# Kernel optimization log

Measured on AMD Instinct MI355X. Metric: run time of the kernel, lower is better.

## Reference

```python
import jax, jax.numpy as jnp
import numpy as np

B, N, M = 16, 4096, 1024
C2, C1 = 256, 128          # points2 channels (in_channel), points1 channels
MLP = [256, 256]
IN0 = C2 + C1              # use_points1=True concat


def setup_inputs() -> dict:
    key = jax.random.key(0)
    ks = jax.random.split(key, 8)
    inp = {
        "xyz1": jax.random.normal(ks[0], (B, 3, N), jnp.float32),
        "xyz2": jax.random.normal(ks[1], (B, 3, M), jnp.float32),
        "points1": jax.random.normal(ks[2], (B, C1, N), jnp.float32),
        "points2": jax.random.normal(ks[3], (B, C2, M), jnp.float32),
        # 1x1 Conv1d weights == dense matrices (out, in)
        "W1": jax.random.normal(ks[4], (MLP[0], IN0), jnp.float32) / np.sqrt(IN0),
        "b1": jnp.zeros((MLP[0],), jnp.float32),
        "W2": jax.random.normal(ks[5], (MLP[1], MLP[0]), jnp.float32) / np.sqrt(MLP[0]),
        "b2": jnp.zeros((MLP[1],), jnp.float32),
    }
    return inp


def _fp(xyz1, xyz2, points1, points2, W1, b1, W2, b2):
    # three_nn: squared pairwise distances via ||a||^2 + ||b||^2 - 2 a.b
    # xyz*: (B, 3, N/M)
    sq1 = jnp.sum(xyz1 * xyz1, axis=1)                 # (B, N)
    sq2 = jnp.sum(xyz2 * xyz2, axis=1)                 # (B, M)
    inner = jnp.einsum("bcn,bcm->bnm", xyz1, xyz2)     # (B, N, M)
    d2 = sq1[:, :, None] + sq2[:, None, :] - 2.0 * inner
    neg_d2, idx = jax.lax.top_k(-d2, 3)                # 3 smallest -> (B, N, 3)
    dist = jnp.sqrt(jnp.maximum(-neg_d2, 1e-20))       # Euclidean, like three_nn wrapper
    dist = jnp.maximum(dist, 1e-10)                    # torch.clamp_min
    recip = 1.0 / dist
    weight = recip / jnp.sum(recip, axis=2, keepdims=True)  # (B, N, 3)
    # three_interpolate: gather points2 at idx and weighted-sum
    gathered = jax.vmap(lambda p, i: p[:, i])(points2, idx)  # (B, C2, N, 3)
    interp = jnp.einsum("bcnk,bnk->bcn", gathered, weight)   # (B, C2, N)
    x = jnp.concatenate([interp, points1], axis=1)           # (B, C2+C1, N)
    # mlp_conv: 1x1 conv + relu (if_bn=False)
    x = jax.nn.relu(jnp.einsum("oc,bcn->bon", W1, x) + b1[None, :, None])
    x = jax.nn.relu(jnp.einsum("oc,bcn->bon", W2, x) + b2[None, :, None])
    return x


def reference(xyz1, xyz2, points1, points2, W1, b1, W2, b2):
    return _fp(xyz1, xyz2, points1, points2, W1, b1, W2, b2)
```

## Files before the change

### kernel.cpp

```cpp
#include <hip/hip_runtime.h>

#define B_  16
#define N_  4096
#define M_  1024
#define C1_ 128
#define C2_ 256
#define K0_ 384
#define O1_ 256
#define O2_ 256

typedef _Float16 half4  __attribute__((ext_vector_type(4)));
typedef _Float16 half8  __attribute__((ext_vector_type(8)));
typedef float    f32x4  __attribute__((ext_vector_type(4)));

__global__ __launch_bounds__(256)
void three_nn_kernel(const float* __restrict__ xyz1, const float* __restrict__ xyz2,
                     int* __restrict__ idxb, float* __restrict__ wb) {
    __shared__ float pts[8 * 516];
    int b = blockIdx.y;
    int t = threadIdx.x;
    {
        const float* src = xyz2 + (size_t)b * 3 * M_;
        int m0 = t * 4;
        f32x4 xv = *(const f32x4*)(src + m0);
        f32x4 yv = *(const f32x4*)(src + M_ + m0);
        f32x4 zv = *(const f32x4*)(src + 2 * M_ + m0);
        float* dst = pts + (m0 >> 7) * 516 + (m0 & 127) * 4;
#pragma unroll
        for (int jj = 0; jj < 4; ++jj) {
            f32x4 o = {xv[jj], yv[jj], zv[jj],
                       fmaf(xv[jj], xv[jj], fmaf(yv[jj], yv[jj], zv[jj] * zv[jj]))};
            *(f32x4*)(dst + jj * 4) = o;
        }
    }
    __syncthreads();
    int lane = t & 63;
    int c = lane & 7;
    int q = ((t >> 6) << 3) + (lane >> 3);
    int n = blockIdx.x * 32 + q;
    const float* qp = xyz1 + (size_t)b * 3 * N_;
    float px = qp[n], py = qp[N_ + n], pz = qp[2 * N_ + n];
    float px2 = -2.f * px, py2 = -2.f * py, pz2 = -2.f * pz;
    const float* base = pts + c * 516;
    float b0 = 1e30f, b1v = 1e30f, b2v = 1e30f;
    int i0 = 0, i1 = 0, i2 = 0;
    int mb = c * 128;
#pragma unroll 4
    for (int i = 0; i < 128; ++i) {
        f32x4 pv = *(const f32x4*)(base + i * 4);
        float d = fmaf(pv[0], px2, fmaf(pv[1], py2, fmaf(pv[2], pz2, pv[3])));
        int m = mb + i;
        bool c0 = d < b0, c1 = d < b1v, c2 = d < b2v;
        float nb1 = __builtin_amdgcn_fmed3f(d, b0, b1v);
        float nb2 = __builtin_amdgcn_fmed3f(d, b1v, b2v);
        i2 = c1 ? i1 : (c2 ? m : i2);
        i1 = c0 ? i0 : (c1 ? m : i1);
        i0 = c0 ? m : i0;
        b0 = fminf(b0, d);
        b1v = nb1; b2v = nb2;
    }
#pragma unroll
    for (int st = 1; st <= 4; st <<= 1) {
        float d0 = __shfl_xor(b0, st, 64);  int j0 = __shfl_xor(i0, st, 64);
        float d1 = __shfl_xor(b1v, st, 64); int j1 = __shfl_xor(i1, st, 64);
        float d2 = __shfl_xor(b2v, st, 64); int j2 = __shfl_xor(i2, st, 64);
#pragma unroll
        for (int e = 0; e < 3; ++e) {
            float d = (e == 0) ? d0 : (e == 1) ? d1 : d2;
            int   m = (e == 0) ? j0 : (e == 1) ? j1 : j2;
            bool c0 = d < b0, c1 = d < b1v, c2 = d < b2v;
            float nb1 = __builtin_amdgcn_fmed3f(d, b0, b1v);
            float nb2 = __builtin_amdgcn_fmed3f(d, b1v, b2v);
            i2 = c1 ? i1 : (c2 ? m : i2);
            i1 = c0 ? i0 : (c1 ? m : i1);
            i0 = c0 ? m : i0;
            b0 = fminf(b0, d);
            b1v = nb1; b2v = nb2;
        }
    }
    if ((lane & 7) == 0) {
        float sq1 = fmaf(px, px, fmaf(py, py, pz * pz));
        float e0 = fmaxf(sqrtf(fmaxf(b0 + sq1, 1e-20f)), 1e-10f);
        float e1 = fmaxf(sqrtf(fmaxf(b1v + sq1, 1e-20f)), 1e-10f);
        float e2 = fmaxf(sqrtf(fmaxf(b2v + sq1, 1e-20f)), 1e-10f);
        float r0 = 1.f / e0, r1 = 1.f / e1, r2 = 1.f / e2;
        float s = r0 + r1 + r2;
        size_t j = ((size_t)b * N_ + n) * 3;
        idxb[j] = i0; idxb[j + 1] = i1; idxb[j + 2] = i2;
        wb[j] = r0 / s; wb[j + 1] = r1 / s; wb[j + 2] = r2 / s;
    }
}

__global__ __launch_bounds__(256)
void convert_w_kernel(const float* __restrict__ W1, const float* __restrict__ W2,
                      _Float16* __restrict__ W1h, _Float16* __restrict__ W2h) {
    int t = blockIdx.x * 256 + threadIdx.x;
    if (t < O1_ * K0_) W1h[t] = (_Float16)W1[t];
    if (t < O2_ * O1_) W2h[t] = (_Float16)W2[t];
}

__global__ __launch_bounds__(256)
void transpose_f16_kernel(const float* __restrict__ in, _Float16* __restrict__ out,
                          int NP, size_t in_bstride, size_t out_bstride,
                          int out_rstride) {
    __shared__ float tile[64][65];
    int t = threadIdx.x;
    int nb = blockIdx.x * 64, cb = blockIdx.y * 64;
    const float* ib = in + blockIdx.z * in_bstride;
#pragma unroll
    for (int r = 0; r < 16; ++r) {
        int cc = r * 4 + (t >> 6);
        tile[cc][t & 63] = ib[(size_t)(cb + cc) * NP + nb + (t & 63)];
    }
    __syncthreads();
    _Float16* ob = out + blockIdx.z * out_bstride;
#pragma unroll
    for (int pass = 0; pass < 2; ++pass) {
        int id = pass * 256 + t;
        int nl = id >> 3;
        int c8 = (id & 7) * 8;
        half8 v;
#pragma unroll
        for (int jj = 0; jj < 8; ++jj) v[jj] = (_Float16)tile[c8 + jj][nl];
        *(half8*)(ob + (size_t)(nb + nl) * out_rstride + cb + c8) = v;
    }
}

__global__ __launch_bounds__(512, 4)
void fused_mlp_kernel(const _Float16* __restrict__ p2T, const int* __restrict__ idxb,
                      const float* __restrict__ wb, const float* __restrict__ points1,
                      const _Float16* __restrict__ p1T,
                      const _Float16* __restrict__ W1h, const float* __restrict__ b1,
                      const _Float16* __restrict__ W2h, const float* __restrict__ b2,
                      float* __restrict__ out) {
    extern __shared__ char smem[];
    char* Xs = smem;
    char* Ys = smem + 64 * 768;
    int b = blockIdx.y;
    int n0b = blockIdx.x * 64;
    int t = threadIdx.x, lane = t & 63, wv = t >> 6;
    int lr = lane & 15, lh = lane >> 4;

    {
        int row = t >> 3, seg = t & 7;
        size_t j = ((size_t)b * N_ + n0b + row) * 3;
        int i0 = idxb[j], i1 = idxb[j + 1], i2 = idxb[j + 2];
        float w0 = wb[j], w1 = wb[j + 1], w2 = wb[j + 2];
        const _Float16* pb = p2T + (size_t)b * M_ * C2_;
        const half8* q0 = (const half8*)(pb + (size_t)i0 * C2_ + seg * 32);
        const half8* q1 = (const half8*)(pb + (size_t)i1 * C2_ + seg * 32);
        const half8* q2 = (const half8*)(pb + (size_t)i2 * C2_ + seg * 32);
        half8 a0[4] = {q0[0], q0[1], q0[2], q0[3]};
        half8 a1[4] = {q1[0], q1[1], q1[2], q1[3]};
        half8 a2[4] = {q2[0], q2[1], q2[2], q2[3]};
        int rswz = (row & 7) << 4;
        char* xrow = Xs + row * 768;
#pragma unroll
        for (int x = 0; x < 4; ++x) {
            half8 v;
#pragma unroll
            for (int jj = 0; jj < 8; ++jj)
                v[jj] = (_Float16)(w0 * (float)a0[x][jj] + w1 * (float)a1[x][jj]
                                 + w2 * (float)a2[x][jj]);
            *(half8*)(xrow + ((seg * 64 + x * 16) ^ rswz)) = v;
        }
        if (p1T) {
            const half8* q3 = (const half8*)(p1T + ((size_t)b * N_ + n0b + row) * C1_ + seg * 16);
            half8 c0v = q3[0], c1v = q3[1];
            *(half8*)(xrow + ((512 + seg * 32) ^ rswz)) = c0v;
            *(half8*)(xrow + ((512 + seg * 32 + 16) ^ rswz)) = c1v;
        } else {
            const float* pp = points1 + ((size_t)b * C1_ + seg * 16) * N_ + n0b + row;
            half8 c0v, c1v;
#pragma unroll
            for (int jj = 0; jj < 8; ++jj) c0v[jj] = (_Float16)pp[(size_t)jj * N_];
#pragma unroll
            for (int jj = 0; jj < 8; ++jj) c1v[jj] = (_Float16)pp[(size_t)(8 + jj) * N_];
            *(half8*)(xrow + ((512 + seg * 32) ^ rswz)) = c0v;
            *(half8*)(xrow + ((512 + seg * 32 + 16) ^ rswz)) = c1v;
        }
    }
    __syncthreads();

    int wvo = wv & 3, wvn = wv >> 2;
    int r0 = wvn * 32 + lr;
    int swz = (r0 & 7) << 4;
    char* x0 = Xs + r0 * 768;
    char* x1 = x0 + 16 * 768;

    f32x4 acc[4][2];
#pragma unroll
    for (int of = 0; of < 4; ++of) {
        int o = wvo * 64 + of * 16 + lh * 4;
        f32x4 bv = {b1[o], b1[o + 1], b1[o + 2], b1[o + 3]};
        acc[of][0] = bv; acc[of][1] = bv;
    }
    const _Float16* w1p = W1h + (size_t)(wvo * 64 + lr) * K0_ + lh * 8;
#pragma unroll
    for (int k0 = 0; k0 < K0_; k0 += 32) {
        half8 bf0 = *(const half8*)(x0 + ((k0 * 2 + lh * 16) ^ swz));
        half8 bf1 = *(const half8*)(x1 + ((k0 * 2 + lh * 16) ^ swz));
#pragma unroll
        for (int of = 0; of < 4; ++of) {
            half8 af = *(const half8*)(w1p + (size_t)of * 16 * K0_ + k0);
            acc[of][0] = __builtin_amdgcn_mfma_f32_16x16x32_f16(af, bf0, acc[of][0], 0, 0, 0);
            acc[of][1] = __builtin_amdgcn_mfma_f32_16x16x32_f16(af, bf1, acc[of][1], 0, 0, 0);
        }
    }
#pragma unroll
    for (int of = 0; of < 4; ++of) {
#pragma unroll
        for (int nf = 0; nf < 2; ++nf) {
            int nrow = wvn * 32 + nf * 16 + lr;
            int obyte = (wvo * 64 + of * 16 + lh * 4) * 2;
            half4 h;
#pragma unroll
            for (int r = 0; r < 4; ++r) h[r] = (_Float16)fmaxf(acc[of][nf][r], 0.f);
            *(half4*)(Ys + ((nrow * 512 + obyte) ^ ((nrow & 7) << 4))) = h;
        }
    }
    __syncthreads();

    f32x4 acc2[4][2];
#pragma unroll
    for (int of = 0; of < 4; ++of) {
        int o = wvo * 64 + of * 16 + lh * 4;
        f32x4 bv = {b2[o], b2[o + 1], b2[o + 2], b2[o + 3]};
        acc2[of][0] = bv; acc2[of][1] = bv;
    }
    const _Float16* w2p = W2h + (size_t)(wvo * 64 + lr) * O1_ + lh * 8;
    char* y0 = Ys + r0 * 512;
    char* y1 = y0 + 16 * 512;
#pragma unroll
    for (int k0 = 0; k0 < O1_; k0 += 32) {
        half8 bb0 = *(const half8*)(y0 + ((k0 * 2 + lh * 16) ^ swz));
        half8 bb1 = *(const half8*)(y1 + ((k0 * 2 + lh * 16) ^ swz));
#pragma unroll
        for (int of = 0; of < 4; ++of) {
            half8 af = *(const half8*)(w2p + (size_t)of * 16 * O1_ + k0);
            acc2[of][0] = __builtin_amdgcn_mfma_f32_16x16x32_f16(af, bb0, acc2[of][0], 0, 0, 0);
            acc2[of][1] = __builtin_amdgcn_mfma_f32_16x16x32_f16(af, bb1, acc2[of][1], 0, 0, 0);
        }
    }
    float* ob = out + (size_t)b * O2_ * N_;
#pragma unroll
    for (int of = 0; of < 4; ++of) {
#pragma unroll
        for (int r = 0; r < 4; ++r) {
            int o2 = wvo * 64 + of * 16 + lh * 4 + r;
#pragma unroll
            for (int nf = 0; nf < 2; ++nf) {
                int n = n0b + wvn * 32 + nf * 16 + lr;
                ob[(size_t)o2 * N_ + n] = fmaxf(acc2[of][nf][r], 0.f);
            }
        }
    }
}

extern "C" void kernel_launch(void* const* d_in, const int* in_sizes, int n_in,
                              void* d_out, int out_size, void* d_ws, size_t ws_size,
                              hipStream_t stream) {
    const float* xyz1    = (const float*)d_in[0];
    const float* xyz2    = (const float*)d_in[1];
    const float* points1 = (const float*)d_in[2];
    const float* points2 = (const float*)d_in[3];
    const float* W1      = (const float*)d_in[4];
    const float* b1      = (const float*)d_in[5];
    const float* W2      = (const float*)d_in[6];
    const float* b2      = (const float*)d_in[7];
    float* out = (float*)d_out;
    (void)in_sizes; (void)n_in; (void)out_size;

    char* p = (char*)d_ws;
    auto alloc = [&](size_t bytes) -> char* {
        char* r = p;
        p += (bytes + 255) & ~(size_t)255;
        return r;
    };
    _Float16* W1h  = (_Float16*)alloc((size_t)O1_ * K0_ * 2);
    _Float16* W2h  = (_Float16*)alloc((size_t)O2_ * O1_ * 2);
    int*      idxb = (int*)alloc((size_t)B_ * N_ * 3 * 4);
    float*    wbuf = (float*)alloc((size_t)B_ * N_ * 3 * 4);
    _Float16* p2T  = (_Float16*)alloc((size_t)B_ * M_ * C2_ * 2);
    size_t used = (size_t)(p - (char*)d_ws);
    size_t p1T_bytes = (size_t)B_ * N_ * C1_ * 2;
    _Float16* p1T = nullptr;
    if (ws_size >= used + p1T_bytes)
        p1T = (_Float16*)alloc(p1T_bytes);

    convert_w_kernel<<<dim3((O1_ * K0_ + 255) / 256), 256, 0, stream>>>(W1, W2, W1h, W2h);
    three_nn_kernel<<<dim3(N_ / 32, B_), 256, 0, stream>>>(xyz1, xyz2, idxb, wbuf);
    transpose_f16_kernel<<<dim3(M_ / 64, C2_ / 64, B_), 256, 0, stream>>>(
        points2, p2T, M_, (size_t)C2_ * M_, (size_t)M_ * C2_, C2_);
    if (p1T)
        transpose_f16_kernel<<<dim3(N_ / 64, C1_ / 64, B_), 256, 0, stream>>>(
            points1, p1T, N_, (size_t)C1_ * N_, (size_t)N_ * C1_, C1_);
    fused_mlp_kernel<<<dim3(N_ / 64, B_), 512, 64 * 768 + 64 * 512, stream>>>(
        p2T, idxb, wbuf, points1, p1T, W1h, b1, W2h, b2, out);
}
```

Baseline: 233.8 us.

## Split fused MLP into two GEMM kernels with fp16 intermediate in workspace

The single fused kernel, which kept the layer-1 activations in shared memory, is split into two kernels. The first does gather, interpolation and GEMM1, then writes ReLU'd fp16 activations to a global workspace buffer. The second reads them back for GEMM2. Each wave now computes a 64x64 tile with 256-thread blocks and no shared-memory Y buffer, which raises register reuse and may change occupancy. The cost is an extra global round trip of B*N*256 fp16 values. If the workspace is too small, the work is chunked over batches, and the p1T transpose is used only when enough workspace remains.

```diff
diff --git a/kernel.cpp b/kernel.cpp
--- a/kernel.cpp
+++ b/kernel.cpp
@@ -126,133 +126,141 @@
     }
 }
 
-__global__ __launch_bounds__(512, 4)
-void fused_mlp_kernel(const _Float16* __restrict__ p2T, const int* __restrict__ idxb,
-                      const float* __restrict__ wb, const float* __restrict__ points1,
-                      const _Float16* __restrict__ p1T,
-                      const _Float16* __restrict__ W1h, const float* __restrict__ b1,
-                      const _Float16* __restrict__ W2h, const float* __restrict__ b2,
-                      float* __restrict__ out) {
-    extern __shared__ char smem[];
-    char* Xs = smem;
-    char* Ys = smem + 64 * 768;
-    int b = blockIdx.y;
+__global__ __launch_bounds__(256, 2)
+void gemm1_fused_kernel(const _Float16* __restrict__ p2T, const int* __restrict__ idxb,
+                        const float* __restrict__ wb, const float* __restrict__ points1,
+                        const _Float16* __restrict__ p1T,
+                        const _Float16* __restrict__ W1h, const float* __restrict__ b1,
+                        _Float16* __restrict__ Y1, int b0) {
+    __shared__ char Xs[64 * 768];
+    int b = b0 + blockIdx.y;
     int n0b = blockIdx.x * 64;
-    int t = threadIdx.x, lane = t & 63, wv = t >> 6;
-    int lr = lane & 15, lh = lane >> 4;
+    int t = threadIdx.x;
 
     {
-        int row = t >> 3, seg = t & 7;
+        int row = t >> 2, sub = t & 3;
         size_t j = ((size_t)b * N_ + n0b + row) * 3;
         int i0 = idxb[j], i1 = idxb[j + 1], i2 = idxb[j + 2];
         float w0 = wb[j], w1 = wb[j + 1], w2 = wb[j + 2];
         const _Float16* pb = p2T + (size_t)b * M_ * C2_;
-        const half8* q0 = (const half8*)(pb + (size_t)i0 * C2_ + seg * 32);
-        const half8* q1 = (const half8*)(pb + (size_t)i1 * C2_ + seg * 32);
-        const half8* q2 = (const half8*)(pb + (size_t)i2 * C2_ + seg * 32);
-        half8 a0[4] = {q0[0], q0[1], q0[2], q0[3]};
-        half8 a1[4] = {q1[0], q1[1], q1[2], q1[3]};
-        half8 a2[4] = {q2[0], q2[1], q2[2], q2[3]};
+        const half8* q0 = (const half8*)(pb + (size_t)i0 * C2_ + sub * 64);
+        const half8* q1 = (const half8*)(pb + (size_t)i1 * C2_ + sub * 64);
+        const half8* q2 = (const half8*)(pb + (size_t)i2 * C2_ + sub * 64);
         int rswz = (row & 7) << 4;
         char* xrow = Xs + row * 768;
 #pragma unroll
-        for (int x = 0; x < 4; ++x) {
+        for (int x = 0; x < 8; ++x) {
+            half8 a0 = q0[x], a1 = q1[x], a2 = q2[x];
             half8 v;
 #pragma unroll
             for (int jj = 0; jj < 8; ++jj)
-                v[jj] = (_Float16)(w0 * (float)a0[x][jj] + w1 * (float)a1[x][jj]
-                                 + w2 * (float)a2[x][jj]);
-            *(half8*)(xrow + ((seg * 64 + x * 16) ^ rswz)) = v;
+                v[jj] = (_Float16)(w0 * (float)a0[jj] + w1 * (float)a1[jj]
+                                 + w2 * (float)a2[jj]);
+            *(half8*)(xrow + ((sub * 128 + x * 16) ^ rswz)) = v;
         }
         if (p1T) {
-            const half8* q3 = (const half8*)(p1T + ((size_t)b * N_ + n0b + row) * C1_ + seg * 16);
-            half8 c0v = q3[0], c1v = q3[1];
-            *(half8*)(xrow + ((512 + seg * 32) ^ rswz)) = c0v;
-            *(half8*)(xrow + ((512 + seg * 32 + 16) ^ rswz)) = c1v;
+            const half8* q3 = (const half8*)(p1T + ((size_t)b * N_ + n0b + row) * C1_ + sub * 32);
+#pragma unroll
+            for (int x = 0; x < 4; ++x) {
+                half8 v = q3[x];
+                *(half8*)(xrow + ((512 + sub * 64 + x * 16) ^ rswz)) = v;
+            }
         } else {
-            const float* pp = points1 + ((size_t)b * C1_ + seg * 16) * N_ + n0b + row;
-            half8 c0v, c1v;
-#pragma unroll
-            for (int jj = 0; jj < 8; ++jj) c0v[jj] = (_Float16)pp[(size_t)jj * N_];
-#pragma unroll
-            for (int jj = 0; jj < 8; ++jj) c1v[jj] = (_Float16)pp[(size_t)(8 + jj) * N_];
-            *(half8*)(xrow + ((512 + seg * 32) ^ rswz)) = c0v;
-            *(half8*)(xrow + ((512 + seg * 32 + 16) ^ rswz)) = c1v;
+            const float* pp = points1 + ((size_t)b * C1_ + sub * 32) * N_ + n0b + row;
+#pragma unroll
+            for (int x = 0; x < 4; ++x) {
+                half8 v;
+#pragma unroll
+                for (int jj = 0; jj < 8; ++jj)
+                    v[jj] = (_Float16)pp[(size_t)(x * 8 + jj) * N_];
+                *(half8*)(xrow + ((512 + sub * 64 + x * 16) ^ rswz)) = v;
+            }
         }
     }
     __syncthreads();
 
-    int wvo = wv & 3, wvn = wv >> 2;
-    int r0 = wvn * 32 + lr;
-    int swz = (r0 & 7) << 4;
-    char* x0 = Xs + r0 * 768;
-    char* x1 = x0 + 16 * 768;
-
-    f32x4 acc[4][2];
+    int lane = t & 63, wv = t >> 6;
+    int lr = lane & 15, lh = lane >> 4;
+    int swz = (lr & 7) << 4;
+
+    f32x4 acc[4][4];
 #pragma unroll
     for (int of = 0; of < 4; ++of) {
-        int o = wvo * 64 + of * 16 + lh * 4;
+        int o = wv * 64 + of * 16 + lh * 4;
         f32x4 bv = {b1[o], b1[o + 1], b1[o + 2], b1[o + 3]};
-        acc[of][0] = bv; acc[of][1] = bv;
-    }
-    const _Float16* w1p = W1h + (size_t)(wvo * 64 + lr) * K0_ + lh * 8;
+#pragma unroll
+        for (int nf = 0; nf < 4; ++nf) acc[of][nf] = bv;
+    }
+    const _Float16* w1p = W1h + (size_t)(wv * 64 + lr) * K0_ + lh * 8;
 #pragma unroll
     for (int k0 = 0; k0 < K0_; k0 += 32) {
-        half8 bf0 = *(const half8*)(x0 + ((k0 * 2 + lh * 16) ^ swz));
-        half8 bf1 = *(const half8*)(x1 + ((k0 * 2 + lh * 16) ^ swz));
+        half8 bf[4];
+#pragma unroll
+        for (int nf = 0; nf < 4; ++nf)
+            bf[nf] = *(const half8*)(Xs + (nf * 16 + lr) * 768 + ((k0 * 2 + lh * 16) ^ swz));
 #pragma unroll
         for (int of = 0; of < 4; ++of) {
             half8 af = *(const half8*)(w1p + (size_t)of * 16 * K0_ + k0);
-            acc[of][0] = __builtin_amdgcn_mfma_f32_16x16x32_f16(af, bf0, acc[of][0], 0, 0, 0);
-            acc[of][1] = __builtin_amdgcn_mfma_f32_16x16x32_f16(af, bf1, acc[of][1], 0, 0, 0);
-        }
-    }
+#pragma unroll
+            for (int nf = 0; nf < 4; ++nf)
+                acc[of][nf] = __builtin_amdgcn_mfma_f32_16x16x32_f16(af, bf[nf], acc[of][nf], 0, 0, 0);
+        }
+    }
+    _Float16* yb = Y1 + ((size_t)b * N_ + n0b) * O1_;
 #pragma unroll
     for (int of = 0; of < 4; ++of) {
 #pragma unroll
-        for (int nf = 0; nf < 2; ++nf) {
-            int nrow = wvn * 32 + nf * 16 + lr;
-            int obyte = (wvo * 64 + of * 16 + lh * 4) * 2;
+        for (int nf = 0; nf < 4; ++nf) {
+            int n = nf * 16 + lr;
+            int o = wv * 64 + of * 16 + lh * 4;
             half4 h;
 #pragma unroll
             for (int r = 0; r < 4; ++r) h[r] = (_Float16)fmaxf(acc[of][nf][r], 0.f);
-            *(half4*)(Ys + ((nrow * 512 + obyte) ^ ((nrow & 7) << 4))) = h;
-        }
-    }
-    __syncthreads();
-
-    f32x4 acc2[4][2];
+            *(half4*)(yb + (size_t)n * O1_ + o) = h;
+        }
+    }
+}
+
+__global__ __launch_bounds__(256, 2)
+void gemm2_kernel(const _Float16* __restrict__ Y1, const _Float16* __restrict__ W2h,
+                  const float* __restrict__ b2, float* __restrict__ out, int b0) {
+    int b = b0 + blockIdx.y;
+    int n0b = blockIdx.x * 64;
+    int t = threadIdx.x, lane = t & 63, wv = t >> 6;
+    int lr = lane & 15, lh = lane >> 4;
+
+    f32x4 acc[4][4];
 #pragma unroll
     for (int of = 0; of < 4; ++of) {
-        int o = wvo * 64 + of * 16 + lh * 4;
+        int o = wv * 64 + of * 16 + lh * 4;
         f32x4 bv = {b2[o], b2[o + 1], b2[o + 2], b2[o + 3]};
-        acc2[of][0] = bv; acc2[of][1] = bv;
-    }
-    const _Float16* w2p = W2h + (size_t)(wvo * 64 + lr) * O1_ + lh * 8;
-    char* y0 = Ys + r0 * 512;
-    char* y1 = y0 + 16 * 512;
+#pragma unroll
+        for (int nf = 0; nf < 4; ++nf) acc[of][nf] = bv;
+    }
+    const _Float16* ap = W2h + (size_t)(wv * 64 + lr) * O1_ + lh * 8;
+    const _Float16* bp = Y1 + ((size_t)b * N_ + n0b + lr) * O1_ + lh * 8;
 #pragma unroll
     for (int k0 = 0; k0 < O1_; k0 += 32) {
-        half8 bb0 = *(const half8*)(y0 + ((k0 * 2 + lh * 16) ^ swz));
-        half8 bb1 = *(const half8*)(y1 + ((k0 * 2 + lh * 16) ^ swz));
-#pragma unroll
-        for (int of = 0; of < 4; ++of) {
-            half8 af = *(const half8*)(w2p + (size_t)of * 16 * O1_ + k0);
-            acc2[of][0] = __builtin_amdgcn_mfma_f32_16x16x32_f16(af, bb0, acc2[of][0], 0, 0, 0);
-            acc2[of][1] = __builtin_amdgcn_mfma_f32_16x16x32_f16(af, bb1, acc2[of][1], 0, 0, 0);
-        }
+        half8 af[4], bf[4];
+#pragma unroll
+        for (int of = 0; of < 4; ++of) af[of] = *(const half8*)(ap + (size_t)of * 16 * O1_ + k0);
+#pragma unroll
+        for (int nf = 0; nf < 4; ++nf) bf[nf] = *(const half8*)(bp + (size_t)nf * 16 * O1_ + k0);
+#pragma unroll
+        for (int of = 0; of < 4; ++of)
+#pragma unroll
+            for (int nf = 0; nf < 4; ++nf)
+                acc[of][nf] = __builtin_amdgcn_mfma_f32_16x16x32_f16(af[of], bf[nf], acc[of][nf], 0, 0, 0);
     }
     float* ob = out + (size_t)b * O2_ * N_;
 #pragma unroll
     for (int of = 0; of < 4; ++of) {
 #pragma unroll
         for (int r = 0; r < 4; ++r) {
-            int o2 = wvo * 64 + of * 16 + lh * 4 + r;
-#pragma unroll
-            for (int nf = 0; nf < 2; ++nf) {
-                int n = n0b + wvn * 32 + nf * 16 + lr;
-                ob[(size_t)o2 * N_ + n] = fmaxf(acc2[of][nf][r], 0.f);
-            }
+            int o2 = wv * 64 + of * 16 + lh * 4 + r;
+#pragma unroll
+            for (int nf = 0; nf < 4; ++nf)
+                ob[(size_t)o2 * N_ + n0b + nf * 16 + lr] = fmaxf(acc[of][nf][r], 0.f);
         }
     }
 }
@@ -282,11 +290,27 @@
     int*      idxb = (int*)alloc((size_t)B_ * N_ * 3 * 4);
     float*    wbuf = (float*)alloc((size_t)B_ * N_ * 3 * 4);
     _Float16* p2T  = (_Float16*)alloc((size_t)B_ * M_ * C2_ * 2);
-    size_t used = (size_t)(p - (char*)d_ws);
+    size_t fixed = (size_t)(p - (char*)d_ws);
+
     size_t p1T_bytes = (size_t)B_ * N_ * C1_ * 2;
+    size_t y1_full   = (size_t)B_ * N_ * O1_ * 2;
+    size_t y1_per_b  = (size_t)N_ * O1_ * 2;
+
     _Float16* p1T = nullptr;
-    if (ws_size >= used + p1T_bytes)
+    _Float16* Y1  = nullptr;
+    int G = B_;
+    if (ws_size >= fixed + p1T_bytes + y1_full) {
         p1T = (_Float16*)alloc(p1T_bytes);
+        Y1  = (_Float16*)alloc(y1_full);
+    } else if (ws_size >= fixed + y1_full) {
+        Y1 = (_Float16*)alloc(y1_full);
+    } else {
+        size_t avail = (ws_size > fixed) ? ws_size - fixed : y1_per_b;
+        G = (int)(avail / y1_per_b);
+        if (G < 1) G = 1;
+        if (G > B_) G = B_;
+        Y1 = (_Float16*)alloc((size_t)G * y1_per_b);
+    }
 
     convert_w_kernel<<<dim3((O1_ * K0_ + 255) / 256), 256, 0, stream>>>(W1, W2, W1h, W2h);
     three_nn_kernel<<<dim3(N_ / 32, B_), 256, 0, stream>>>(xyz1, xyz2, idxb, wbuf);
@@ -295,6 +319,17 @@
     if (p1T)
         transpose_f16_kernel<<<dim3(N_ / 64, C1_ / 64, B_), 256, 0, stream>>>(
             points1, p1T, N_, (size_t)C1_ * N_, (size_t)N_ * C1_, C1_);
-    fused_mlp_kernel<<<dim3(N_ / 64, B_), 512, 64 * 768 + 64 * 512, stream>>>(
-        p2T, idxb, wbuf, points1, p1T, W1h, b1, W2h, b2, out);
-}
+
+    if (G >= B_) {
+        gemm1_fused_kernel<<<dim3(N_ / 64, B_), 256, 0, stream>>>(
+            p2T, idxb, wbuf, points1, p1T, W1h, b1, Y1, 0);
+        gemm2_kernel<<<dim3(N_ / 64, B_), 256, 0, stream>>>(Y1, W2h, b2, out, 0);
+    } else {
+        for (int b0 = 0; b0 < B_; b0 += G) {
+            int gc = (B_ - b0 < G) ? (B_ - b0) : G;
+            gemm1_fused_kernel<<<dim3(N_ / 64, gc), 256, 0, stream>>>(
+                p2T, idxb, wbuf, points1, p1T, W1h, b1, Y1, b0);
+            gemm2_kernel<<<dim3(N_ / 64, gc), 256, 0, stream>>>(Y1, W2h, b2, out, b0);
+        }
+    }
+}
```

New measurement: 234.7 us. No clear change (+0.4%).
